# Optimization experiments

Measured on AMD Instinct MI355X. Metric: run time of the kernel, lower is better.

The kernel has to match this reference:

```python
import jax, jax.numpy as jnp
import numpy as np

HIDDEN = 4096
SPARSITY_RATIO = 0.1
BLOCK_SIZE = max(1, int(HIDDEN * SPARSITY_RATIO * 2))  # 819, matches torch block_diagonal


def _block_diag_mask(h: int, block_size: int) -> jnp.ndarray:
    # mask[i, j] = True iff i and j fall in the same diagonal block of size block_size
    # (last block may be partial) -- equivalent to the torch loop via floor division
    idx = jnp.arange(h) // block_size
    return idx[:, None] == idx[None, :]


def setup_inputs() -> dict:
    key = jax.random.key(0)
    kx, kw = jax.random.split(key)
    x = jax.random.normal(kx, (8, 2048, HIDDEN), dtype=jnp.float32)
    mask = _block_diag_mask(HIDDEN, BLOCK_SIZE)
    eye = jnp.eye(HIDDEN, dtype=jnp.float32)
    W = eye + 0.1 * jax.random.normal(kw, (HIDDEN, HIDDEN), dtype=jnp.float32)
    # replicate torch init: masked noise on-pattern, identity off-pattern
    W = W * mask.astype(jnp.float32) + eye * (~mask).astype(jnp.float32)
    return {"x": x, "W": W, "mask": mask}


def reference(x, W, mask):
    sparse_W = W * mask.astype(W.dtype)           # [H, H]
    return jnp.einsum('bsh,oh->bso', x, sparse_W)  # x @ sparse_W.T
```

## Files before the change

kernel.cpp:

```cpp
#include <hip/hip_runtime.h>
#include <hip/hip_bf16.h>

#define H       4096
#define BS      819
#define NB      5
#define KPAD    832
#define NPAD    896
#define M_TOTAL 16384
#define XB_LD   (NB * KPAD)

typedef __bf16 bf16x8 __attribute__((ext_vector_type(8)));
typedef float  f32x4  __attribute__((ext_vector_type(4)));

__device__ __forceinline__ void gld_lds16(const void* gptr, void* ldsptr) {
    __builtin_amdgcn_global_load_lds(
        (const __attribute__((address_space(1))) void*)gptr,
        (__attribute__((address_space(3))) void*)ldsptr,
        16, 0, 0);
}

__global__ void pack_x_kernel(const float* __restrict__ x,
                              __hip_bfloat16* __restrict__ xb) {
    const int m  = blockIdx.y;
    const int j4 = (blockIdx.x * blockDim.x + threadIdx.x) * 4;
    if (j4 >= XB_LD) return;
    const int g  = j4 / KPAD;
    const int jj = j4 - g * KPAD;
    const float* xr = x + (size_t)m * H + g * BS;
    union { __hip_bfloat16 h[4]; uint2 u; } v;
#pragma unroll
    for (int i = 0; i < 4; ++i) {
        float f = (jj + i < BS) ? xr[jj + i] : 0.f;
        v.h[i] = __float2bfloat16(f);
    }
    *reinterpret_cast<uint2*>(xb + (size_t)m * XB_LD + j4) = v.u;
}

__global__ void pack_w_kernel(const float* __restrict__ W,
                              __hip_bfloat16* __restrict__ wb) {
    const int g   = blockIdx.y;
    const int idx = blockIdx.x * blockDim.x + threadIdx.x;
    if (idx >= NPAD * KPAD) return;
    const int n = idx / KPAD;
    const int k = idx - n * KPAD;
    float v = 0.f;
    if (n < BS && k < BS)
        v = W[(size_t)(g * BS + n) * H + g * BS + k];
    wb[(size_t)g * NPAD * KPAD + idx] = __float2bfloat16(v);
}

__global__ void last_col_kernel(const float* __restrict__ x,
                                const float* __restrict__ W,
                                float* __restrict__ out) {
    const int m = blockIdx.x * blockDim.x + threadIdx.x;
    if (m >= M_TOTAL) return;
    const float w = W[(size_t)4095 * H + 4095];
    out[(size_t)m * H + 4095] = x[(size_t)m * H + 4095] * w;
}

__global__ void gemm_kernel(const __hip_bfloat16* __restrict__ xb,
                            const __hip_bfloat16* __restrict__ wb,
                            float* __restrict__ out) {
    __shared__ __hip_bfloat16 lA[128 * 32];
    __shared__ __hip_bfloat16 lB[128 * 32];

    const int tid   = threadIdx.x;
    const int mBase = blockIdx.x * 128;
    const int nBase = blockIdx.y * 128;
    const int g     = blockIdx.z;
    const int lane  = tid & 63;
    const int wave  = tid >> 6;
    const int waveM = wave >> 1;
    const int waveN = wave & 1;
    const int quad  = lane >> 4;
    const int l16   = lane & 15;

    const int c0 = tid,        r0 = c0 >> 2, kq0 = (c0 & 3) * 8;
    const int c1 = tid + 256,  r1 = c1 >> 2, kq1 = (c1 & 3) * 8;

    const __hip_bfloat16* a0 = xb + (size_t)(mBase + r0) * XB_LD + (size_t)g * KPAD + kq0;
    const __hip_bfloat16* a1 = xb + (size_t)(mBase + r1) * XB_LD + (size_t)g * KPAD + kq1;
    const __hip_bfloat16* b0 = wb + ((size_t)g * NPAD + nBase + r0) * KPAD + kq0;
    const __hip_bfloat16* b1 = wb + ((size_t)g * NPAD + nBase + r1) * KPAD + kq1;

    char* lAb = (char*)lA;
    char* lBb = (char*)lB;

    f32x4 acc[4][4] = {};

    for (int kt = 0; kt < KPAD / 32; ++kt) {
        const int k0 = kt * 32;
        gld_lds16(a0 + k0, lAb + c0 * 16);
        gld_lds16(a1 + k0, lAb + c1 * 16);
        gld_lds16(b0 + k0, lBb + c0 * 16);
        gld_lds16(b1 + k0, lBb + c1 * 16);
        __syncthreads();

        bf16x8 a[4], b[4];
#pragma unroll
        for (int mi = 0; mi < 4; ++mi)
            a[mi] = *reinterpret_cast<const bf16x8*>(lA + (waveM * 64 + mi * 16 + l16) * 32 + quad * 8);
#pragma unroll
        for (int ni = 0; ni < 4; ++ni)
            b[ni] = *reinterpret_cast<const bf16x8*>(lB + (waveN * 64 + ni * 16 + l16) * 32 + quad * 8);

#pragma unroll
        for (int mi = 0; mi < 4; ++mi)
#pragma unroll
            for (int ni = 0; ni < 4; ++ni)
                acc[mi][ni] = __builtin_amdgcn_mfma_f32_16x16x32_bf16(a[mi], b[ni], acc[mi][ni], 0, 0, 0);
        __syncthreads();
    }

#pragma unroll
    for (int mi = 0; mi < 4; ++mi) {
        const int mrow = mBase + waveM * 64 + mi * 16 + quad * 4;
#pragma unroll
        for (int ni = 0; ni < 4; ++ni) {
            const int ncol = nBase + waveN * 64 + ni * 16 + l16;
            if (ncol < BS) {
                float* op = out + (size_t)mrow * H + (size_t)g * BS + ncol;
#pragma unroll
                for (int r = 0; r < 4; ++r)
                    op[(size_t)r * H] = acc[mi][ni][r];
            }
        }
    }
}

__global__ void fallback_kernel(const float* __restrict__ x,
                                const float* __restrict__ W,
                                float* __restrict__ out) {
    const size_t idx = (size_t)blockIdx.x * blockDim.x + threadIdx.x;
    if (idx >= (size_t)M_TOTAL * H) return;
    const int m = (int)(idx / H);
    const int o = (int)(idx % H);
    const int g = o / BS;
    const int h0 = g * BS;
    const int len = (g < NB) ? BS : 1;
    const float* xr = x + (size_t)m * H + h0;
    const float* wr = W + (size_t)o * H + h0;
    float s = 0.f;
    for (int k = 0; k < len; ++k) s += xr[k] * wr[k];
    out[idx] = s;
}

extern "C" void kernel_launch(void* const* d_in, const int* in_sizes, int n_in,
                              void* d_out, int out_size, void* d_ws, size_t ws_size,
                              hipStream_t stream) {
    const float* x = (const float*)d_in[0];
    const float* W = (const float*)d_in[1];
    float* out = (float*)d_out;

    const size_t xb_elems = (size_t)M_TOTAL * XB_LD;
    const size_t wb_elems = (size_t)NB * NPAD * KPAD;
    const size_t need = (xb_elems + wb_elems) * sizeof(__hip_bfloat16);

    if (ws_size < need) {
        const size_t total = (size_t)M_TOTAL * H;
        fallback_kernel<<<(unsigned)((total + 255) / 256), 256, 0, stream>>>(x, W, out);
        return;
    }

    __hip_bfloat16* xb = (__hip_bfloat16*)d_ws;
    __hip_bfloat16* wb = xb + xb_elems;

    pack_x_kernel<<<dim3((XB_LD / 4 + 255) / 256, M_TOTAL), 256, 0, stream>>>(x, xb);
    pack_w_kernel<<<dim3((NPAD * KPAD + 255) / 256, NB), 256, 0, stream>>>(W, wb);
    gemm_kernel<<<dim3(M_TOTAL / 128, NPAD / 128, NB), 256, 0, stream>>>(xb, wb, out);
    last_col_kernel<<<(M_TOTAL + 255) / 256, 256, 0, stream>>>(x, W, out);
}
```

Before: 685.6 us.

## Fuse prep kernels and rewrite GEMM with 256x256 tiles and multi-stage LDS pipeline

Merges the x packing, W packing and last-column kernels into one prep launch with wider vectorized loads. The GEMM moves to 256x256 tiles with 512 threads and a 4-buffer LDS ring that prefetches two stages ahead, using explicit vmcnt waits instead of a double __syncthreads. It also adds an XOR swizzle on LDS chunks to avoid bank conflicts and raises wave priority around the MFMA block. The goal is to hide global-load latency and cut per-launch overhead, at the cost of more LDS and registers per block. The larger N tile also computes more padding past the 819-column block.

```diff
diff --git a/kernel.cpp b/kernel.cpp
--- a/kernel.cpp
+++ b/kernel.cpp
@@ -5,12 +5,16 @@
 #define BS      819
 #define NB      5
 #define KPAD    832
-#define NPAD    896
+#define NPADW   896
 #define M_TOTAL 16384
 #define XB_LD   (NB * KPAD)
+#define NT      (KPAD / 32)
+#define BM      256
+#define BN      256
 
 typedef __bf16 bf16x8 __attribute__((ext_vector_type(8)));
 typedef float  f32x4  __attribute__((ext_vector_type(4)));
+typedef float  f32x4u __attribute__((ext_vector_type(4), aligned(4)));
 
 __device__ __forceinline__ void gld_lds16(const void* gptr, void* ldsptr) {
     __builtin_amdgcn_global_load_lds(
@@ -19,107 +23,163 @@
         16, 0, 0);
 }
 
-__global__ void pack_x_kernel(const float* __restrict__ x,
-                              __hip_bfloat16* __restrict__ xb) {
-    const int m  = blockIdx.y;
-    const int j4 = (blockIdx.x * blockDim.x + threadIdx.x) * 4;
-    if (j4 >= XB_LD) return;
-    const int g  = j4 / KPAD;
-    const int jj = j4 - g * KPAD;
-    const float* xr = x + (size_t)m * H + g * BS;
-    union { __hip_bfloat16 h[4]; uint2 u; } v;
-#pragma unroll
-    for (int i = 0; i < 4; ++i) {
-        float f = (jj + i < BS) ? xr[jj + i] : 0.f;
-        v.h[i] = __float2bfloat16(f);
-    }
-    *reinterpret_cast<uint2*>(xb + (size_t)m * XB_LD + j4) = v.u;
-}
-
-__global__ void pack_w_kernel(const float* __restrict__ W,
-                              __hip_bfloat16* __restrict__ wb) {
-    const int g   = blockIdx.y;
-    const int idx = blockIdx.x * blockDim.x + threadIdx.x;
-    if (idx >= NPAD * KPAD) return;
-    const int n = idx / KPAD;
-    const int k = idx - n * KPAD;
-    float v = 0.f;
-    if (n < BS && k < BS)
-        v = W[(size_t)(g * BS + n) * H + g * BS + k];
-    wb[(size_t)g * NPAD * KPAD + idx] = __float2bfloat16(v);
-}
-
-__global__ void last_col_kernel(const float* __restrict__ x,
-                                const float* __restrict__ W,
-                                float* __restrict__ out) {
-    const int m = blockIdx.x * blockDim.x + threadIdx.x;
-    if (m >= M_TOTAL) return;
-    const float w = W[(size_t)4095 * H + 4095];
-    out[(size_t)m * H + 4095] = x[(size_t)m * H + 4095] * w;
-}
-
-__global__ void gemm_kernel(const __hip_bfloat16* __restrict__ xb,
-                            const __hip_bfloat16* __restrict__ wb,
+#define PX_GX     3
+#define PX_BLOCKS (PX_GX * M_TOTAL)
+#define PW_PER_G  ((NPADW * KPAD) / 4 / 256)
+#define PW_BLOCKS (PW_PER_G * NB)
+#define LC_BLOCKS (M_TOTAL / 256)
+
+__global__ void prep_kernel(const float* __restrict__ x,
+                            const float* __restrict__ W,
+                            __hip_bfloat16* __restrict__ xb,
+                            __hip_bfloat16* __restrict__ wb,
                             float* __restrict__ out) {
-    __shared__ __hip_bfloat16 lA[128 * 32];
-    __shared__ __hip_bfloat16 lB[128 * 32];
-
-    const int tid   = threadIdx.x;
-    const int mBase = blockIdx.x * 128;
-    const int nBase = blockIdx.y * 128;
+    const int bid = blockIdx.x;
+    if (bid < PX_BLOCKS) {
+        const int m  = bid / PX_GX;
+        const int c8 = (bid % PX_GX) * 256 + threadIdx.x;
+        if (c8 >= XB_LD / 8) return;
+        const int j8 = c8 * 8;
+        const int g  = j8 / KPAD;
+        const int jj = j8 - g * KPAD;
+        const float* xr = x + (size_t)m * H + g * BS;
+        union { __hip_bfloat16 h[8]; uint4 u; } v;
+        if (jj + 8 <= BS) {
+            f32x4u f0 = *reinterpret_cast<const f32x4u*>(xr + jj);
+            f32x4u f1 = *reinterpret_cast<const f32x4u*>(xr + jj + 4);
+#pragma unroll
+            for (int i = 0; i < 4; ++i) {
+                v.h[i]     = __float2bfloat16(f0[i]);
+                v.h[4 + i] = __float2bfloat16(f1[i]);
+            }
+        } else {
+#pragma unroll
+            for (int i = 0; i < 8; ++i) {
+                float f = (jj + i < BS) ? xr[jj + i] : 0.f;
+                v.h[i] = __float2bfloat16(f);
+            }
+        }
+        *reinterpret_cast<uint4*>(xb + (size_t)m * XB_LD + j8) = v.u;
+    } else if (bid < PX_BLOCKS + PW_BLOCKS) {
+        const int b   = bid - PX_BLOCKS;
+        const int g   = b / PW_PER_G;
+        const int t4  = (b - g * PW_PER_G) * 256 + threadIdx.x;
+        const int idx = t4 * 4;
+        const int n = idx / KPAD;
+        const int k = idx - n * KPAD;
+        union { __hip_bfloat16 h[4]; uint2 u; } v;
+        if (n < BS && k + 4 <= BS) {
+            f32x4u f = *reinterpret_cast<const f32x4u*>(W + (size_t)(g * BS + n) * H + g * BS + k);
+#pragma unroll
+            for (int i = 0; i < 4; ++i) v.h[i] = __float2bfloat16(f[i]);
+        } else {
+#pragma unroll
+            for (int i = 0; i < 4; ++i) {
+                float f = 0.f;
+                if (n < BS && k + i < BS) f = W[(size_t)(g * BS + n) * H + g * BS + k + i];
+                v.h[i] = __float2bfloat16(f);
+            }
+        }
+        *reinterpret_cast<uint2*>(wb + ((size_t)g * NPADW + n) * KPAD + k) = v.u;
+    } else {
+        const int m = (bid - PX_BLOCKS - PW_BLOCKS) * 256 + threadIdx.x;
+        if (m >= M_TOTAL) return;
+        const float w = W[(size_t)4095 * H + 4095];
+        out[(size_t)m * H + 4095] = x[(size_t)m * H + 4095] * w;
+    }
+}
+
+__global__ __launch_bounds__(512, 2)
+void gemm_kernel(const __hip_bfloat16* __restrict__ xb,
+                 const __hip_bfloat16* __restrict__ wb,
+                 float* __restrict__ out) {
+    __shared__ __hip_bfloat16 sA[4][BM * 32];
+    __shared__ __hip_bfloat16 sB[4][BN * 32];
+
+    const int tid  = threadIdx.x;
+    const int lane = tid & 63;
+    const int wid  = tid >> 6;
+    const int wr   = wid >> 2;
+    const int wc   = wid & 3;
+    const int l16  = lane & 15;
+    const int quad = lane >> 4;
+
+    const int mBase = blockIdx.x * BM;
+    const int nBase = blockIdx.y * BN;
     const int g     = blockIdx.z;
-    const int lane  = tid & 63;
-    const int wave  = tid >> 6;
-    const int waveM = wave >> 1;
-    const int waveN = wave & 1;
-    const int quad  = lane >> 4;
-    const int l16   = lane & 15;
-
-    const int c0 = tid,        r0 = c0 >> 2, kq0 = (c0 & 3) * 8;
-    const int c1 = tid + 256,  r1 = c1 >> 2, kq1 = (c1 & 3) * 8;
-
-    const __hip_bfloat16* a0 = xb + (size_t)(mBase + r0) * XB_LD + (size_t)g * KPAD + kq0;
-    const __hip_bfloat16* a1 = xb + (size_t)(mBase + r1) * XB_LD + (size_t)g * KPAD + kq1;
-    const __hip_bfloat16* b0 = wb + ((size_t)g * NPAD + nBase + r0) * KPAD + kq0;
-    const __hip_bfloat16* b1 = wb + ((size_t)g * NPAD + nBase + r1) * KPAD + kq1;
-
-    char* lAb = (char*)lA;
-    char* lBb = (char*)lB;
-
-    f32x4 acc[4][4] = {};
-
-    for (int kt = 0; kt < KPAD / 32; ++kt) {
-        const int k0 = kt * 32;
-        gld_lds16(a0 + k0, lAb + c0 * 16);
-        gld_lds16(a1 + k0, lAb + c1 * 16);
-        gld_lds16(b0 + k0, lBb + c0 * 16);
-        gld_lds16(b1 + k0, lBb + c1 * 16);
-        __syncthreads();
-
-        bf16x8 a[4], b[4];
-#pragma unroll
-        for (int mi = 0; mi < 4; ++mi)
-            a[mi] = *reinterpret_cast<const bf16x8*>(lA + (waveM * 64 + mi * 16 + l16) * 32 + quad * 8);
+
+    const int r0 = tid >> 2;
+    const int kc = (tid & 3) ^ ((tid >> 3) & 3);
+
+    const __hip_bfloat16* aSrc0 = xb + (size_t)(mBase + r0      ) * XB_LD + g * KPAD + kc * 8;
+    const __hip_bfloat16* aSrc1 = xb + (size_t)(mBase + r0 + 128) * XB_LD + g * KPAD + kc * 8;
+    int nrow0 = nBase + r0;        if (nrow0 > NPADW - 1) nrow0 = NPADW - 1;
+    int nrow1 = nBase + r0 + 128;  if (nrow1 > NPADW - 1) nrow1 = NPADW - 1;
+    const __hip_bfloat16* bSrc0 = wb + ((size_t)g * NPADW + nrow0) * KPAD + kc * 8;
+    const __hip_bfloat16* bSrc1 = wb + ((size_t)g * NPADW + nrow1) * KPAD + kc * 8;
+
+    const int dst0 = tid * 16;
+    const int dst1 = dst0 + 8192;
+
+    const int cpr  = quad ^ ((l16 >> 1) & 3);
+    const int aOff = (wr * 128 + l16) * 32 + cpr * 8;
+    const int bOff = (wc * 64  + l16) * 32 + cpr * 8;
+
+    f32x4 acc[8][4] = {};
+
+#define STAGE(t, buf) do {                                       \
+        const int koff = (t) * 32;                               \
+        gld_lds16(aSrc0 + koff, (char*)sA[(buf)] + dst0);        \
+        gld_lds16(aSrc1 + koff, (char*)sA[(buf)] + dst1);        \
+        gld_lds16(bSrc0 + koff, (char*)sB[(buf)] + dst0);        \
+        gld_lds16(bSrc1 + koff, (char*)sB[(buf)] + dst1);        \
+    } while (0)
+
+    STAGE(0, 0);
+    STAGE(1, 1);
+
+    for (int t = 0; t < NT; ++t) {
+        if (t + 2 < NT) STAGE(t + 2, (t + 2) & 3);
+        __builtin_amdgcn_sched_barrier(0);
+        if (t + 2 < NT) {
+            asm volatile("s_waitcnt vmcnt(8)" ::: "memory");
+        } else if (t + 1 < NT) {
+            asm volatile("s_waitcnt vmcnt(4)" ::: "memory");
+        } else {
+            asm volatile("s_waitcnt vmcnt(0)" ::: "memory");
+        }
+        __builtin_amdgcn_s_barrier();
+        __builtin_amdgcn_sched_barrier(0);
+
+        const __hip_bfloat16* A = sA[t & 3];
+        const __hip_bfloat16* B = sB[t & 3];
+        bf16x8 a[8], b[4];
 #pragma unroll
         for (int ni = 0; ni < 4; ++ni)
-            b[ni] = *reinterpret_cast<const bf16x8*>(lB + (waveN * 64 + ni * 16 + l16) * 32 + quad * 8);
-
-#pragma unroll
-        for (int mi = 0; mi < 4; ++mi)
+            b[ni] = *reinterpret_cast<const bf16x8*>(B + bOff + ni * 512);
+#pragma unroll
+        for (int mi = 0; mi < 8; ++mi)
+            a[mi] = *reinterpret_cast<const bf16x8*>(A + aOff + mi * 512);
+
+        __builtin_amdgcn_s_setprio(1);
+#pragma unroll
+        for (int mi = 0; mi < 8; ++mi)
 #pragma unroll
             for (int ni = 0; ni < 4; ++ni)
                 acc[mi][ni] = __builtin_amdgcn_mfma_f32_16x16x32_bf16(a[mi], b[ni], acc[mi][ni], 0, 0, 0);
-        __syncthreads();
-    }
-
-#pragma unroll
-    for (int mi = 0; mi < 4; ++mi) {
-        const int mrow = mBase + waveM * 64 + mi * 16 + quad * 4;
+        __builtin_amdgcn_s_setprio(0);
+    }
+#undef STAGE
+
+    const int orow0 = mBase + wr * 128 + quad * 4;
+    const int ocol0 = nBase + wc * 64 + l16;
+#pragma unroll
+    for (int mi = 0; mi < 8; ++mi) {
 #pragma unroll
         for (int ni = 0; ni < 4; ++ni) {
-            const int ncol = nBase + waveN * 64 + ni * 16 + l16;
-            if (ncol < BS) {
-                float* op = out + (size_t)mrow * H + (size_t)g * BS + ncol;
+            const int nc = ocol0 + ni * 16;
+            if (nc < BS) {
+                float* op = out + (size_t)(orow0 + mi * 16) * H + (size_t)g * BS + nc;
 #pragma unroll
                 for (int r = 0; r < 4; ++r)
                     op[(size_t)r * H] = acc[mi][ni][r];
@@ -153,7 +213,7 @@
     float* out = (float*)d_out;
 
     const size_t xb_elems = (size_t)M_TOTAL * XB_LD;
-    const size_t wb_elems = (size_t)NB * NPAD * KPAD;
+    const size_t wb_elems = (size_t)NB * NPADW * KPAD;
     const size_t need = (xb_elems + wb_elems) * sizeof(__hip_bfloat16);
 
     if (ws_size < need) {
@@ -165,8 +225,6 @@
     __hip_bfloat16* xb = (__hip_bfloat16*)d_ws;
     __hip_bfloat16* wb = xb + xb_elems;
 
-    pack_x_kernel<<<dim3((XB_LD / 4 + 255) / 256, M_TOTAL), 256, 0, stream>>>(x, xb);
-    pack_w_kernel<<<dim3((NPAD * KPAD + 255) / 256, NB), 256, 0, stream>>>(W, wb);
-    gemm_kernel<<<dim3(M_TOTAL / 128, NPAD / 128, NB), 256, 0, stream>>>(xb, wb, out);
-    last_col_kernel<<<(M_TOTAL + 255) / 256, 256, 0, stream>>>(x, W, out);
-}
+    prep_kernel<<<PX_BLOCKS + PW_BLOCKS + LC_BLOCKS, 256, 0, stream>>>(x, W, xb, wb, out);
+    gemm_kernel<<<dim3(M_TOTAL / BM, 4, NB), 512, 0, stream>>>(xb, wb, out);
+}
```

New measurement: 662.4 us. 3.4% less time.
